# Performance work log

Measured on AMD Instinct MI355X. Metric: run time of the kernel, lower is better.

## Reference

```python
import jax, jax.numpy as jnp
import numpy as np

B, T, C, H = 4, 2048, 1024, 16
D = C // H          # head_dim = 64
FF = 2 * C          # ff_mult = 2
EPS = 1e-5


def _layernorm(x, g, b):
    mu = jnp.mean(x, axis=-1, keepdims=True)
    var = jnp.mean((x - mu) ** 2, axis=-1, keepdims=True)
    return (x - mu) * jax.lax.rsqrt(var + EPS) * g + b


def setup_inputs() -> dict:
    key = jax.random.key(0)
    ks = jax.random.split(key, 8)
    x = jax.random.normal(ks[0], (B, T, C), dtype=jnp.float32)
    perm = jax.random.permutation(ks[1], T).astype(jnp.int32)
    s_c = 1.0 / np.sqrt(C)
    s_f = 1.0 / np.sqrt(FF)
    Wqkv = jax.random.normal(ks[2], (C, 3 * C), dtype=jnp.float32) * s_c
    Wproj = jax.random.normal(ks[3], (C, C), dtype=jnp.float32) * s_c
    bproj = jnp.zeros((C,), dtype=jnp.float32)
    ln1_g = jnp.ones((C,), dtype=jnp.float32)
    ln1_b = jnp.zeros((C,), dtype=jnp.float32)
    ln2_g = jnp.ones((C,), dtype=jnp.float32)
    ln2_b = jnp.zeros((C,), dtype=jnp.float32)
    Wff1 = jax.random.normal(ks[4], (C, FF), dtype=jnp.float32) * s_c
    bff1 = jnp.zeros((FF,), dtype=jnp.float32)
    Wff2 = jax.random.normal(ks[5], (FF, C), dtype=jnp.float32) * s_f
    bff2 = jnp.zeros((C,), dtype=jnp.float32)
    return {"x": x, "perm": perm, "Wqkv": Wqkv, "Wproj": Wproj, "bproj": bproj,
            "ln1_g": ln1_g, "ln1_b": ln1_b, "ln2_g": ln2_g, "ln2_b": ln2_b,
            "Wff1": Wff1, "bff1": bff1, "Wff2": Wff2, "bff2": bff2}


def reference(x, perm, Wqkv, Wproj, bproj, ln1_g, ln1_b, ln2_g, ln2_b,
              Wff1, bff1, Wff2, bff2):
    # --- attention branch ---
    h = _layernorm(x, ln1_g, ln1_b)                       # [B,T,C]
    qkv = (h @ Wqkv).reshape(B, T, 3, H, D)
    q, k, v = qkv[:, :, 0], qkv[:, :, 1], qkv[:, :, 2]    # [B,T,H,D]
    # random-permuted causal additive mask: masked = ~tril[:, perm]
    rows = jnp.arange(T)[:, None]
    masked = perm[None, :] > rows                          # [T,T] bool
    bias = jnp.where(masked, -jnp.inf, 0.0).astype(x.dtype)
    scale = 1.0 / np.sqrt(D)
    scores = jnp.einsum('bqhd,bkhd->bhqk', q, k) * scale + bias
    attn = jax.nn.softmax(scores, axis=-1)                 # [B,H,T,T]
    y = jnp.einsum('bhqk,bkhd->bqhd', attn, v).reshape(B, T, C)
    x = x + y @ Wproj + bproj
    # --- MLP branch ---
    h2 = _layernorm(x, ln2_g, ln2_b)
    ff = jax.nn.gelu(h2 @ Wff1 + bff1, approximate=False) @ Wff2 + bff2
    return x + ff
```

## Files before the change

### kernel.cpp

```cpp
#include <hip/hip_runtime.h>
#include <math.h>

#define Bb 4
#define Tt 2048
#define Cc 1024
#define Hh 16
#define Dd 64
#define FFf 2048
#define Mrows (Bb*Tt)

typedef _Float16 f16;
typedef _Float16 half8 __attribute__((ext_vector_type(8)));
typedef _Float16 half4 __attribute__((ext_vector_type(4)));
typedef _Float16 half2 __attribute__((ext_vector_type(2)));
typedef float floatx4 __attribute__((ext_vector_type(4)));

#define MFMA16(a,b,c)    __builtin_amdgcn_mfma_f32_16x16x32_f16(a,b,c,0,0,0)
#define MFMA16K16(a,b,c) __builtin_amdgcn_mfma_f32_16x16x16f16(a,b,c,0,0,0)

__device__ __forceinline__ void g2l16(const void* g, void* l) {
  __builtin_amdgcn_global_load_lds((__attribute__((address_space(1))) void*)(g),
                                   (__attribute__((address_space(3))) void*)(l),
                                   16, 0, 0);
}

__global__ __launch_bounds__(256) void wt_kernel(const float* __restrict__ W,
                                                 f16* __restrict__ WT,
                                                 const int K, const int N) {
  __shared__ float tile[32][33];
  const int n0 = blockIdx.x * 32, k0 = blockIdx.y * 32;
  const int tx = threadIdx.x, ty = threadIdx.y;
  #pragma unroll
  for (int i = 0; i < 4; i++)
    tile[ty + 8*i][tx] = W[(size_t)(k0 + ty + 8*i) * N + n0 + tx];
  __syncthreads();
  #pragma unroll
  for (int i = 0; i < 4; i++)
    WT[(size_t)(n0 + ty + 8*i) * K + k0 + tx] = (f16)tile[tx][ty + 8*i];
}

__global__ __launch_bounds__(256) void ln_kernel(const float* __restrict__ x,
                                                 const float* __restrict__ gam,
                                                 const float* __restrict__ bet,
                                                 f16* __restrict__ out) {
  const int row = blockIdx.x;
  const int tid = threadIdx.x;
  const float4 v = ((const float4*)(x + (size_t)row * Cc))[tid];
  float s  = v.x + v.y + v.z + v.w;
  float ss = v.x*v.x + v.y*v.y + v.z*v.z + v.w*v.w;
  #pragma unroll
  for (int o = 32; o >= 1; o >>= 1) { s += __shfl_xor(s, o); ss += __shfl_xor(ss, o); }
  __shared__ float ps[4], pss[4];
  if ((tid & 63) == 0) { ps[tid >> 6] = s; pss[tid >> 6] = ss; }
  __syncthreads();
  s  = ps[0] + ps[1] + ps[2] + ps[3];
  ss = pss[0] + pss[1] + pss[2] + pss[3];
  const float mu   = s * (1.0f / Cc);
  const float rstd = rsqrtf(ss * (1.0f / Cc) - mu * mu + 1e-5f);
  const float4 g4 = ((const float4*)gam)[tid];
  const float4 b4 = ((const float4*)bet)[tid];
  half4 o;
  o[0] = (f16)((v.x - mu) * rstd * g4.x + b4.x);
  o[1] = (f16)((v.y - mu) * rstd * g4.y + b4.y);
  o[2] = (f16)((v.z - mu) * rstd * g4.z + b4.z);
  o[3] = (f16)((v.w - mu) * rstd * g4.w + b4.w);
  ((half4*)(out + (size_t)row * Cc))[tid] = o;
}

template <int MODE>
__global__ __launch_bounds__(256, 2) void gemm_kernel(
    const f16* __restrict__ A, const f16* __restrict__ Bt, const int Kdim,
    const float* __restrict__ resid, const float* __restrict__ bias,
    float* __restrict__ outF, f16* __restrict__ outH,
    f16* __restrict__ outQ, f16* __restrict__ outK, f16* __restrict__ outV) {
  __shared__ f16 As[128 * 32];
  __shared__ f16 Bs[128 * 32];
  const int tid = threadIdx.x;
  const int lane = tid & 63;
  const int w = tid >> 6;
  const int wr = w >> 1, wc = w & 1;
  const int bm = blockIdx.y, bn = blockIdx.x;

  floatx4 acc[4][4] = {};

  const size_t aBase = (size_t)(bm*128 + w*32 + (lane >> 2)) * Kdim + (lane & 3) * 8;
  const size_t bBase = (size_t)(bn*128 + w*32 + (lane >> 2)) * Kdim + (lane & 3) * 8;

  for (int ks = 0; ks < Kdim; ks += 32) {
    __syncthreads();
    g2l16(A  + aBase + ks,                    &As[(w*2 + 0) * 512]);
    g2l16(A  + aBase + (size_t)16*Kdim + ks,  &As[(w*2 + 1) * 512]);
    g2l16(Bt + bBase + ks,                    &Bs[(w*2 + 0) * 512]);
    g2l16(Bt + bBase + (size_t)16*Kdim + ks,  &Bs[(w*2 + 1) * 512]);
    __syncthreads();
    half8 aF[4], bF[4];
    #pragma unroll
    for (int mi = 0; mi < 4; mi++)
      aF[mi] = *(const half8*)&As[(wr*64 + mi*16 + (lane & 15)) * 32 + (lane >> 4) * 8];
    #pragma unroll
    for (int ni = 0; ni < 4; ni++)
      bF[ni] = *(const half8*)&Bs[(wc*64 + ni*16 + (lane & 15)) * 32 + (lane >> 4) * 8];
    #pragma unroll
    for (int mi = 0; mi < 4; mi++)
      #pragma unroll
      for (int ni = 0; ni < 4; ni++)
        acc[mi][ni] = MFMA16(aF[mi], bF[ni], acc[mi][ni]);
  }

  const int rowBase = bm*128 + wr*64;
  const int colBase = bn*128 + wc*64;
  const int quadL = (lane >> 4);
  #pragma unroll
  for (int mi = 0; mi < 4; mi++) {
    #pragma unroll
    for (int ni = 0; ni < 4; ni++) {
      const int col = colBase + ni*16 + (lane & 15);
      if (MODE == 0) {
        const int s = col >> 10;
        const int hh = (col >> 6) & 15;
        const int d = col & 63;
        const int row0 = rowBase + mi*16 + quadL*4;
        const int bI = row0 >> 11;
        const int t0 = row0 & 2047;
        if (s == 2) {
          const size_t addr = (((size_t)(bI*Hh + hh)) * Dd + d) * Tt +
                              (t0 & ~63) + quadL*16 + ((t0 >> 4) & 3) * 4;
          half4 o;
          #pragma unroll
          for (int r = 0; r < 4; r++) o[r] = (f16)acc[mi][ni][r];
          *(half4*)&outV[addr] = o;
        } else {
          f16* dst = (s == 0) ? outQ : outK;
          const float sc = (s == 0) ? 0.18033688f : 1.0f;
          #pragma unroll
          for (int r = 0; r < 4; r++)
            dst[(((size_t)(bI*Hh + hh)) * Tt + t0 + r) * Dd + d] = (f16)(acc[mi][ni][r] * sc);
        }
      } else {
        #pragma unroll
        for (int r = 0; r < 4; r++) {
          const int row = rowBase + mi*16 + quadL*4 + r;
          const float vv = acc[mi][ni][r];
          if (MODE == 1) {
            const size_t a = (size_t)row * Cc + col;
            outF[a] = vv + resid[a] + bias[col];
          } else if (MODE == 2) {
            const float t = vv + bias[col];
            const float gl = 0.5f * t * (1.0f + erff(t * 0.70710678118654752f));
            outH[(size_t)row * FFf + col] = (f16)gl;
          } else {
            const size_t a = (size_t)row * Cc + col;
            outF[a] = vv + bias[col] + resid[a];
          }
        }
      }
    }
  }
}

__global__ __launch_bounds__(256, 4) void attn_kernel(
    const f16* __restrict__ Q, const f16* __restrict__ Kg,
    const f16* __restrict__ Vtp, const int* __restrict__ perm,
    f16* __restrict__ Y) {
  __shared__ f16 Ks[64 * 64];
  __shared__ f16 Vs[64 * 64];
  __shared__ int permS[64];

  const int tid = threadIdx.x;
  const int lane = tid & 63;
  const int w = tid >> 6;
  const int low = lane & 15;
  const int quad = lane >> 4;
  const int bh = blockIdx.y;
  const int q0 = blockIdx.x * 128;
  const int b = bh >> 4, h = bh & 15;

  half8 qF[2][2];
  {
    const size_t base = ((size_t)bh * Tt + q0 + w*32) * Dd;
    #pragma unroll
    for (int qi = 0; qi < 2; qi++)
      #pragma unroll
      for (int kc = 0; kc < 2; kc++)
        qF[qi][kc] = *(const half8*)(Q + base + (size_t)(qi*16 + low) * Dd +
                                     kc*32 + quad*8);
  }

  floatx4 O[4][2] = {};
  float l_[2] = {0.f, 0.f};

  const int gd = ((lane & 7) ^ (lane >> 3)) * 8;
  const int krow = lane >> 3;

  for (int kt = 0; kt < Tt / 64; kt++) {
    const int kbase = kt * 64;
    __syncthreads();
    {
      const size_t kgBase = ((size_t)bh * Tt + kbase) * Dd;
      const size_t vgBase = ((size_t)bh * Dd) * Tt + kbase;
      g2l16(Kg  + kgBase + (size_t)(w*16 + 0 + krow) * Dd + gd, &Ks[(w*2 + 0) * 512]);
      g2l16(Kg  + kgBase + (size_t)(w*16 + 8 + krow) * Dd + gd, &Ks[(w*2 + 1) * 512]);
      g2l16(Vtp + vgBase + (size_t)(w*16 + 0 + krow) * Tt + gd, &Vs[(w*2 + 0) * 512]);
      g2l16(Vtp + vgBase + (size_t)(w*16 + 8 + krow) * Tt + gd, &Vs[(w*2 + 1) * 512]);
      if (tid < 64) permS[tid] = perm[kbase + tid];
    }
    __syncthreads();

    floatx4 S[2][4] = {};
    #pragma unroll
    for (int kc = 0; kc < 2; kc++) {
      #pragma unroll
      for (int ki = 0; ki < 4; ki++) {
        const int key = ki*16 + low;
        const half8 kf = *(const half8*)&Ks[key * 64 + (((kc*4 + quad) ^ (lane & 7)) * 8)];
        S[0][ki] = MFMA16(kf, qF[0][kc], S[0][ki]);
        S[1][ki] = MFMA16(kf, qF[1][kc], S[1][ki]);
      }
    }

    int4 pk[4];
    #pragma unroll
    for (int ki = 0; ki < 4; ki++) pk[ki] = *(const int4*)&permS[ki*16 + quad*4];

    half4 pF[2][4];
    #pragma unroll
    for (int qi = 0; qi < 2; qi++) {
      const int qrow = q0 + w*32 + qi*16 + low;
      #pragma unroll
      for (int ki = 0; ki < 4; ki++) {
        const floatx4 sv = S[qi][ki];
        const float p0 = (pk[ki].x > qrow) ? 0.f : __builtin_amdgcn_exp2f(sv[0]);
        const float p1 = (pk[ki].y > qrow) ? 0.f : __builtin_amdgcn_exp2f(sv[1]);
        const float p2 = (pk[ki].z > qrow) ? 0.f : __builtin_amdgcn_exp2f(sv[2]);
        const float p3 = (pk[ki].w > qrow) ? 0.f : __builtin_amdgcn_exp2f(sv[3]);
        l_[qi] += (p0 + p1) + (p2 + p3);
        const half2 lo = __builtin_bit_cast(half2, __builtin_amdgcn_cvt_pkrtz(p0, p1));
        const half2 hi = __builtin_bit_cast(half2, __builtin_amdgcn_cvt_pkrtz(p2, p3));
        pF[qi][ki] = __builtin_shufflevector(lo, hi, 0, 1, 2, 3);
      }
    }

    #pragma unroll
    for (int ki2 = 0; ki2 < 2; ki2++) {
      #pragma unroll
      for (int ni = 0; ni < 4; ni++) {
        const int d = ni*16 + low;
        const half8 v8 = *(const half8*)&Vs[d * 64 + (((quad*2 + ki2) ^ (lane & 7)) * 8)];
        const half4 vfA = __builtin_shufflevector(v8, v8, 0, 1, 2, 3);
        const half4 vfB = __builtin_shufflevector(v8, v8, 4, 5, 6, 7);
        O[ni][0] = MFMA16K16(vfA, pF[0][2*ki2 + 0], O[ni][0]);
        O[ni][1] = MFMA16K16(vfA, pF[1][2*ki2 + 0], O[ni][1]);
        O[ni][0] = MFMA16K16(vfB, pF[0][2*ki2 + 1], O[ni][0]);
        O[ni][1] = MFMA16K16(vfB, pF[1][2*ki2 + 1], O[ni][1]);
      }
    }
  }

  #pragma unroll
  for (int qi = 0; qi < 2; qi++) {
    l_[qi] += __shfl_xor(l_[qi], 16);
    l_[qi] += __shfl_xor(l_[qi], 32);
  }

  #pragma unroll
  for (int qi = 0; qi < 2; qi++) {
    const float linv = 1.0f / l_[qi];
    const int trow = q0 + w*32 + qi*16 + low;
    #pragma unroll
    for (int ni = 0; ni < 4; ni++) {
      half4 o;
      #pragma unroll
      for (int r = 0; r < 4; r++) o[r] = (f16)(O[ni][qi][r] * linv);
      *(half4*)&Y[((size_t)(b * Tt + trow)) * Cc + h*64 + ni*16 + quad*4] = o;
    }
  }
}

extern "C" void kernel_launch(void* const* d_in, const int* in_sizes, int n_in,
                              void* d_out, int out_size, void* d_ws, size_t ws_size,
                              hipStream_t stream) {
  const float* x     = (const float*)d_in[0];
  const int*   perm  = (const int*)d_in[1];
  const float* Wqkv  = (const float*)d_in[2];
  const float* Wproj = (const float*)d_in[3];
  const float* bproj = (const float*)d_in[4];
  const float* ln1g  = (const float*)d_in[5];
  const float* ln1b  = (const float*)d_in[6];
  const float* ln2g  = (const float*)d_in[7];
  const float* ln2b  = (const float*)d_in[8];
  const float* Wff1  = (const float*)d_in[9];
  const float* bff1  = (const float*)d_in[10];
  const float* Wff2  = (const float*)d_in[11];
  const float* bff2  = (const float*)d_in[12];
  float* out = (float*)d_out;

  char* ws = (char*)d_ws;
  size_t off = 0;
  auto alloc = [&](size_t bytes) -> void* {
    void* p = ws + off;
    off += (bytes + 255) & ~(size_t)255;
    return p;
  };
  f16*   h1     = (f16*)alloc((size_t)Mrows * Cc * 2);
  f16*   qb     = (f16*)alloc((size_t)Mrows * Cc * 2);
  f16*   kb     = (f16*)alloc((size_t)Mrows * Cc * 2);
  f16*   vtp    = (f16*)alloc((size_t)Mrows * Cc * 2);
  f16*   yb     = (f16*)alloc((size_t)Mrows * Cc * 2);
  float* xa     = (float*)alloc((size_t)Mrows * Cc * 4);
  f16*   h2     = (f16*)alloc((size_t)Mrows * Cc * 2);
  f16*   gb     = (f16*)alloc((size_t)Mrows * FFf * 2);
  f16*   WqkvT  = (f16*)alloc((size_t)3 * Cc * Cc * 2);
  f16*   WprojT = (f16*)alloc((size_t)Cc * Cc * 2);
  f16*   Wff1T  = (f16*)alloc((size_t)FFf * Cc * 2);
  f16*   Wff2T  = (f16*)alloc((size_t)Cc * FFf * 2);

  const dim3 blkT(32, 8);
  wt_kernel<<<dim3(3*Cc/32, Cc/32), blkT, 0, stream>>>(Wqkv,  WqkvT,  Cc,  3*Cc);
  wt_kernel<<<dim3(Cc/32,   Cc/32), blkT, 0, stream>>>(Wproj, WprojT, Cc,  Cc);
  wt_kernel<<<dim3(FFf/32,  Cc/32), blkT, 0, stream>>>(Wff1,  Wff1T,  Cc,  FFf);
  wt_kernel<<<dim3(Cc/32,  FFf/32), blkT, 0, stream>>>(Wff2,  Wff2T,  FFf, Cc);

  ln_kernel<<<Mrows, 256, 0, stream>>>(x, ln1g, ln1b, h1);

  gemm_kernel<0><<<dim3(3*Cc/128, Mrows/128), 256, 0, stream>>>(
      h1, WqkvT, Cc, nullptr, nullptr, nullptr, nullptr, qb, kb, vtp);

  attn_kernel<<<dim3(Tt/128, Bb*Hh), 256, 0, stream>>>(qb, kb, vtp, perm, yb);

  gemm_kernel<1><<<dim3(Cc/128, Mrows/128), 256, 0, stream>>>(
      yb, WprojT, Cc, x, bproj, xa, nullptr, nullptr, nullptr, nullptr);

  ln_kernel<<<Mrows, 256, 0, stream>>>(xa, ln2g, ln2b, h2);

  gemm_kernel<2><<<dim3(FFf/128, Mrows/128), 256, 0, stream>>>(
      h2, Wff1T, Cc, nullptr, bff1, nullptr, gb, nullptr, nullptr, nullptr);

  gemm_kernel<3><<<dim3(Cc/128, Mrows/128), 256, 0, stream>>>(
      gb, Wff2T, FFf, xa, bff2, out, nullptr, nullptr, nullptr, nullptr);
}
```

Measured before the change: 450.5 us.

## Merge weight transposes, raise GEMM occupancy, compute softmax row sums via MFMA

Fuses the four weight-transpose launches into a single kernel that dispatches on block index, which removes launch overhead. It raises the GEMM launch-bounds occupancy hint from 2 to 3 blocks per CU, which can force register spilling. In attention it replaces the scalar per-lane row-sum accumulation and cross-lane shuffles with an MFMA against a ones vector. The row sum then comes from the matrix unit, computed from the fp16-rounded probabilities.

```diff
diff --git a/kernel.cpp b/kernel.cpp
--- a/kernel.cpp
+++ b/kernel.cpp
@@ -24,11 +24,18 @@
                                    16, 0, 0);
 }
 
-__global__ __launch_bounds__(256) void wt_kernel(const float* __restrict__ W,
-                                                 f16* __restrict__ WT,
-                                                 const int K, const int N) {
+__global__ __launch_bounds__(256) void wt_all_kernel(
+    const float* __restrict__ Wqkv, const float* __restrict__ Wproj,
+    const float* __restrict__ Wff1, const float* __restrict__ Wff2,
+    f16* __restrict__ WqkvT, f16* __restrict__ WprojT,
+    f16* __restrict__ Wff1T, f16* __restrict__ Wff2T) {
   __shared__ float tile[32][33];
-  const int n0 = blockIdx.x * 32, k0 = blockIdx.y * 32;
+  int idx = blockIdx.x;
+  const float* W; f16* WT; int K, N, n0, k0;
+  if (idx < 3072)      { W = Wqkv;  WT = WqkvT;  K = Cc;  N = 3*Cc; n0 = (idx % 96)*32; k0 = (idx / 96)*32; }
+  else if (idx < 4096) { idx -= 3072; W = Wproj; WT = WprojT; K = Cc;  N = Cc;  n0 = (idx % 32)*32; k0 = (idx / 32)*32; }
+  else if (idx < 6144) { idx -= 4096; W = Wff1;  WT = Wff1T;  K = Cc;  N = FFf; n0 = (idx % 64)*32; k0 = (idx / 64)*32; }
+  else                 { idx -= 6144; W = Wff2;  WT = Wff2T;  K = FFf; N = Cc;  n0 = (idx % 32)*32; k0 = (idx / 32)*32; }
   const int tx = threadIdx.x, ty = threadIdx.y;
   #pragma unroll
   for (int i = 0; i < 4; i++)
@@ -68,7 +75,7 @@
 }
 
 template <int MODE>
-__global__ __launch_bounds__(256, 2) void gemm_kernel(
+__global__ __launch_bounds__(256, 3) void gemm_kernel(
     const f16* __restrict__ A, const f16* __restrict__ Bt, const int Kdim,
     const float* __restrict__ resid, const float* __restrict__ bias,
     float* __restrict__ outF, f16* __restrict__ outH,
@@ -187,7 +194,8 @@
   }
 
   floatx4 O[4][2] = {};
-  float l_[2] = {0.f, 0.f};
+  floatx4 Ol[2] = {};
+  const half4 ones4 = {(f16)1.f, (f16)1.f, (f16)1.f, (f16)1.f};
 
   const int gd = ((lane & 7) ^ (lane >> 3)) * 8;
   const int krow = lane >> 3;
@@ -233,7 +241,6 @@
         const float p1 = (pk[ki].y > qrow) ? 0.f : __builtin_amdgcn_exp2f(sv[1]);
         const float p2 = (pk[ki].z > qrow) ? 0.f : __builtin_amdgcn_exp2f(sv[2]);
         const float p3 = (pk[ki].w > qrow) ? 0.f : __builtin_amdgcn_exp2f(sv[3]);
-        l_[qi] += (p0 + p1) + (p2 + p3);
         const half2 lo = __builtin_bit_cast(half2, __builtin_amdgcn_cvt_pkrtz(p0, p1));
         const half2 hi = __builtin_bit_cast(half2, __builtin_amdgcn_cvt_pkrtz(p2, p3));
         pF[qi][ki] = __builtin_shufflevector(lo, hi, 0, 1, 2, 3);
@@ -242,6 +249,10 @@
 
     #pragma unroll
     for (int ki2 = 0; ki2 < 2; ki2++) {
+      Ol[0] = MFMA16K16(ones4, pF[0][2*ki2 + 0], Ol[0]);
+      Ol[1] = MFMA16K16(ones4, pF[1][2*ki2 + 0], Ol[1]);
+      Ol[0] = MFMA16K16(ones4, pF[0][2*ki2 + 1], Ol[0]);
+      Ol[1] = MFMA16K16(ones4, pF[1][2*ki2 + 1], Ol[1]);
       #pragma unroll
       for (int ni = 0; ni < 4; ni++) {
         const int d = ni*16 + low;
@@ -258,13 +269,7 @@
 
   #pragma unroll
   for (int qi = 0; qi < 2; qi++) {
-    l_[qi] += __shfl_xor(l_[qi], 16);
-    l_[qi] += __shfl_xor(l_[qi], 32);
-  }
-
-  #pragma unroll
-  for (int qi = 0; qi < 2; qi++) {
-    const float linv = 1.0f / l_[qi];
+    const float linv = 1.0f / Ol[qi][0];
     const int trow = q0 + w*32 + qi*16 + low;
     #pragma unroll
     for (int ni = 0; ni < 4; ni++) {
@@ -314,11 +319,8 @@
   f16*   Wff1T  = (f16*)alloc((size_t)FFf * Cc * 2);
   f16*   Wff2T  = (f16*)alloc((size_t)Cc * FFf * 2);
 
-  const dim3 blkT(32, 8);
-  wt_kernel<<<dim3(3*Cc/32, Cc/32), blkT, 0, stream>>>(Wqkv,  WqkvT,  Cc,  3*Cc);
-  wt_kernel<<<dim3(Cc/32,   Cc/32), blkT, 0, stream>>>(Wproj, WprojT, Cc,  Cc);
-  wt_kernel<<<dim3(FFf/32,  Cc/32), blkT, 0, stream>>>(Wff1,  Wff1T,  Cc,  FFf);
-  wt_kernel<<<dim3(Cc/32,  FFf/32), blkT, 0, stream>>>(Wff2,  Wff2T,  FFf, Cc);
+  wt_all_kernel<<<8192, dim3(32, 8), 0, stream>>>(Wqkv, Wproj, Wff1, Wff2,
+                                                  WqkvT, WprojT, Wff1T, Wff2T);
 
   ln_kernel<<<Mrows, 256, 0, stream>>>(x, ln1g, ln1b, h1);
 
```

Result: no change. 446.1 us (-1.0%).
